# Kernel optimization log

Measured on AMD Instinct MI355X. Metric: run time of the kernel, lower is better.

## Reference

```python
import math
import jax, jax.numpy as jnp
import numpy as np

N_HEADS = 16
LOCAL_HEADS = 8
GLOBAL_HEADS = N_HEADS - LOCAL_HEADS
WINDOW = 256
NEG_INF = -1e30


def setup_inputs() -> dict:
    key = jax.random.key(0)
    ks = jax.random.split(key, 6)
    B, S, E = 1, 4096, 1024
    inp = {
        "hidden_states": jax.random.normal(ks[0], (B, S, E), dtype=jnp.float32),
        "Wq": jax.random.normal(ks[1], (E, E), dtype=jnp.float32) * (1.0 / math.sqrt(E)),
        "Wk": jax.random.normal(ks[2], (E, E), dtype=jnp.float32) * (1.0 / math.sqrt(E)),
        "Wv": jax.random.normal(ks[3], (E, E), dtype=jnp.float32) * (1.0 / math.sqrt(E)),
        "Wo": jax.random.normal(ks[4], (E, E), dtype=jnp.float32) * (1.0 / math.sqrt(E)),
        "bo": jnp.zeros((E,), dtype=jnp.float32),
    }
    return inp


def reference(hidden_states, Wq, Wk, Wv, Wo, bo):
    B, S, E = hidden_states.shape
    H, D = N_HEADS, E // N_HEADS
    scale = 1.0 / math.sqrt(D)

    def proj(W):
        # nn.Linear: x @ W.T ; reshape to [B, H, S, D]
        y = jnp.einsum('bse,fe->bsf', hidden_states, W)
        return y.reshape(B, S, H, D).transpose(0, 2, 1, 3)

    q = proj(Wq) * scale
    k = proj(Wk)
    v = proj(Wv)

    i = jnp.arange(S)[:, None]
    j = jnp.arange(S)[None, :]
    causal = j <= i                      # [S, S] allowed positions
    local = causal & (j >= i - WINDOW)   # sliding window of width WINDOW+1

    def attend(qh, kh, vh, mask):
        scores = jnp.einsum('bhsd,bhtd->bhst', qh, kh)
        scores = jnp.where(mask, scores, NEG_INF)
        w = jax.nn.softmax(scores, axis=-1)
        return jnp.einsum('bhst,bhtd->bhsd', w, vh)

    out_g = attend(q[:, :GLOBAL_HEADS], k[:, :GLOBAL_HEADS], v[:, :GLOBAL_HEADS], causal)
    out_l = attend(q[:, GLOBAL_HEADS:], k[:, GLOBAL_HEADS:], v[:, GLOBAL_HEADS:], local)

    attn = jnp.concatenate([out_g, out_l], axis=1)       # [B, H, S, D]
    attn = attn.transpose(0, 2, 1, 3).reshape(B, S, E)    # [B, S, E]
    return jnp.einsum('bse,fe->bsf', attn, Wo) + bo
```

## Files before the change

### kernel.cpp

```cpp
#include <hip/hip_runtime.h>
#include <hip/hip_fp16.h>

#define S_LEN 4096
#define EMB   1024
#define NH    16
#define HD    64
#define GH    8
#define WIN   256

typedef _Float16 half8 __attribute__((ext_vector_type(8)));
typedef float    f32x4 __attribute__((ext_vector_type(4)));
typedef unsigned short ushort8 __attribute__((ext_vector_type(8)));

static __device__ __forceinline__ f32x4 mfma16(half8 a, half8 b, f32x4 c) {
    return __builtin_amdgcn_mfma_f32_16x16x32_f16(a, b, c, 0, 0, 0);
}

#define GLOAD16(g, l) __builtin_amdgcn_global_load_lds( \
    (const __attribute__((address_space(1))) void*)(g), \
    (__attribute__((address_space(3))) void*)(l), 16, 0, 0)

__global__ __launch_bounds__(256) void split_kernel(
    const float* __restrict__ X,  const float* __restrict__ Wq, const float* __restrict__ Wk,
    const float* __restrict__ Wv, const float* __restrict__ Wo,
    __half* __restrict__ Xhi, __half* __restrict__ Xlo,
    __half* __restrict__ Wh,  __half* __restrict__ Wl,
    __half* __restrict__ Woh, __half* __restrict__ Wol)
{
    const int NT = gridDim.x * blockDim.x;
    for (int i = blockIdx.x * blockDim.x + threadIdx.x; i < 2097152; i += NT) {
        const float* src; __half *dh, *dl; int off;
        if (i < 1048576)      { src = X;  dh = Xhi;           dl = Xlo;           off = i; }
        else if (i < 1310720) { src = Wq; dh = Wh;            dl = Wl;            off = i - 1048576; }
        else if (i < 1572864) { src = Wk; dh = Wh + 1048576;  dl = Wl + 1048576;  off = i - 1310720; }
        else if (i < 1835008) { src = Wv; dh = Wh + 2097152;  dl = Wl + 2097152;  off = i - 1572864; }
        else                  { src = Wo; dh = Woh;           dl = Wol;           off = i - 1835008; }
        float4 xv = *(const float4*)(src + (size_t)off * 4);
        union { __half h[4]; uint2 u; } ph, pl;
        float xs[4] = {xv.x, xv.y, xv.z, xv.w};
        #pragma unroll
        for (int j = 0; j < 4; ++j) {
            __half hj = __float2half_rn(xs[j]);
            ph.h[j] = hj;
            pl.h[j] = __float2half_rn(xs[j] - __half2float(hj));
        }
        *(uint2*)(dh + (size_t)off * 4) = ph.u;
        *(uint2*)(dl + (size_t)off * 4) = pl.u;
    }
}

__global__ __launch_bounds__(256) void gemm_split_kernel(
    const __half* __restrict__ Ah_, const __half* __restrict__ Al_,
    const __half* __restrict__ Bh_, const __half* __restrict__ Bl_,
    int mode, __half* __restrict__ qkv_out,
    float* __restrict__ fo_out, const float* __restrict__ bias)
{
    __shared__ __align__(16) char lds[65536];
    char* LA_h = lds;
    char* LA_l = lds + 16384;
    char* LB_h = lds + 32768;
    char* LB_l = lds + 49152;

    const int tid  = threadIdx.x;
    const int w    = tid >> 6, lane = tid & 63;
    const int bm   = blockIdx.x * 128, bn = blockIdx.y * 128;
    const int wm0  = (w & 1) * 64, wn0 = (w >> 1) * 64;
    const int lr   = lane & 15;
    const int lk   = lane >> 4;

    const char *gAh[4], *gAl[4], *gBh[4], *gBl[4];
    int ldsoff[4];
    #pragma unroll
    for (int i = 0; i < 4; ++i) {
        const int c = tid + i * 256;
        const int row = c >> 3;
        const int sw  = ((c & 7) ^ (row & 7)) * 16;
        gAh[i] = (const char*)Ah_ + (size_t)(bm + row) * 2048 + sw;
        gAl[i] = (const char*)Al_ + (size_t)(bm + row) * 2048 + sw;
        gBh[i] = (const char*)Bh_ + (size_t)(bn + row) * 2048 + sw;
        gBl[i] = (const char*)Bl_ + (size_t)(bn + row) * 2048 + sw;
        ldsoff[i] = ((tid >> 6) * 64 + i * 256) * 16;
    }

    f32x4 acc[4][4];
    #pragma unroll
    for (int mi = 0; mi < 4; ++mi)
        #pragma unroll
        for (int ni = 0; ni < 4; ++ni) acc[mi][ni] = (f32x4){0.f, 0.f, 0.f, 0.f};

    for (int k0 = 0; k0 < 1024; k0 += 64) {
        __syncthreads();
        const size_t kb = (size_t)k0 * 2;
        #pragma unroll
        for (int i = 0; i < 4; ++i) {
            GLOAD16(gAh[i] + kb, LA_h + ldsoff[i]);
            GLOAD16(gAl[i] + kb, LA_l + ldsoff[i]);
            GLOAD16(gBh[i] + kb, LB_h + ldsoff[i]);
            GLOAD16(gBl[i] + kb, LB_l + ldsoff[i]);
        }
        __syncthreads();

        #pragma unroll
        for (int kh = 0; kh < 2; ++kh) {
            half8 afh[4], afl[4], bfh[4], bfl[4];
            #pragma unroll
            for (int f = 0; f < 4; ++f) {
                const int ar = wm0 + f * 16 + lr;
                const int ab = ar * 128 + ((kh * 64 + lk * 16) ^ ((ar & 7) << 4));
                afh[f] = *(const half8*)(LA_h + ab);
                afl[f] = *(const half8*)(LA_l + ab);
                const int br = wn0 + f * 16 + lr;
                const int bb = br * 128 + ((kh * 64 + lk * 16) ^ ((br & 7) << 4));
                bfh[f] = *(const half8*)(LB_h + bb);
                bfl[f] = *(const half8*)(LB_l + bb);
            }
            #pragma unroll
            for (int mi = 0; mi < 4; ++mi)
                #pragma unroll
                for (int ni = 0; ni < 4; ++ni) {
                    acc[mi][ni] = mfma16(afh[mi], bfh[ni], acc[mi][ni]);
                    acc[mi][ni] = mfma16(afh[mi], bfl[ni], acc[mi][ni]);
                    acc[mi][ni] = mfma16(afl[mi], bfh[ni], acc[mi][ni]);
                }
        }
    }

    if (mode == 0) {
        #pragma unroll
        for (int ni = 0; ni < 4; ++ni) {
            const int n  = bn + wn0 + ni * 16 + lr;
            const int hg = n >> 6;
            const int d  = n & 63;
            const float alpha = ((n >> 10) == 0) ? 0.125f : 1.0f;
            __half* base = qkv_out + (size_t)hg * S_LEN * HD + d;
            #pragma unroll
            for (int mi = 0; mi < 4; ++mi) {
                const int m = bm + wm0 + mi * 16 + lk * 4;
                #pragma unroll
                for (int r = 0; r < 4; ++r)
                    base[(size_t)(m + r) * HD] = __float2half_rn(acc[mi][ni][r] * alpha);
            }
        }
    } else {
        #pragma unroll
        for (int ni = 0; ni < 4; ++ni) {
            const int n = bn + wn0 + ni * 16 + lr;
            const float bv = bias[n];
            #pragma unroll
            for (int mi = 0; mi < 4; ++mi) {
                const int m = bm + wm0 + mi * 16 + lk * 4;
                #pragma unroll
                for (int r = 0; r < 4; ++r)
                    fo_out[(size_t)(m + r) * EMB + n] = acc[mi][ni][r] + bv;
            }
        }
    }
}

__global__ __launch_bounds__(256) void attn_mfma_kernel(
    const __half* __restrict__ q, const __half* __restrict__ k, const __half* __restrict__ v,
    __half* __restrict__ Ohi, __half* __restrict__ Olo )
{
    __shared__ __align__(16) unsigned char smem[32768];
    char* Qs = (char*)smem;
    char* Ks = (char*)smem + 8192;
    char* Vt = (char*)smem + 16384;
    char* Pl = (char*)smem + 24576;

    const int qb  = 63 - blockIdx.x;
    const int h   = blockIdx.y;
    const bool is_local = (h >= GH);
    const int tid  = threadIdx.x;
    const int w    = tid >> 6;
    const int lane = tid & 63;
    const int lq   = lane & 15;
    const int hi   = lane >> 4;

    const char* qh = (const char*)(q + (size_t)h * S_LEN * HD);
    const char* kh = (const char*)(k + (size_t)h * S_LEN * HD);
    const char* vh = (const char*)(v + (size_t)h * S_LEN * HD);

    #pragma unroll
    for (int e = 0; e < 2; ++e) {
        const int flat = e * 4096 + tid * 16;
        const int row  = flat >> 7;
        const int src  = flat ^ ((row & 7) << 4);
        *(uint4*)(Qs + flat) = *(const uint4*)(qh + (size_t)qb * 8192 + src);
    }
    __syncthreads();

    half8 qf[2];
    #pragma unroll
    for (int ks = 0; ks < 2; ++ks) {
        const int row = w * 16 + lq;
        int byte = row * 128 + hi * 16 + ks * 64;
        byte ^= (row & 7) << 4;
        qf[ks] = *(const half8*)(Qs + byte);
    }

    float m_run = -1e30f, l_run = 0.f;
    f32x4 po[4];
    #pragma unroll
    for (int i = 0; i < 4; ++i) po[i] = (f32x4){0.f, 0.f, 0.f, 0.f};

    const int qg = qb * 64 + w * 16 + lq;
    const int kt_lo = is_local ? ((qb - 4 > 0) ? qb - 4 : 0) : 0;
    char* plw = Pl + w * 2048;

    for (int kv = kt_lo; kv <= qb; ++kv) {
        __syncthreads();

        #pragma unroll
        for (int e = 0; e < 2; ++e) {
            const int flat = e * 4096 + tid * 16;
            const int row  = flat >> 7;
            const int src  = flat ^ ((row & 7) << 4);
            *(uint4*)(Ks + flat) = *(const uint4*)(kh + (size_t)kv * 8192 + src);
        }
        {
            const int j0 = (tid & 31) * 2;
            const int d0 = (tid >> 5) * 8;
            ushort8 v0 = *(const ushort8*)(vh + (size_t)(kv * 64 + j0)     * 128 + d0 * 2);
            ushort8 v1 = *(const ushort8*)(vh + (size_t)(kv * 64 + j0 + 1) * 128 + d0 * 2);
            #pragma unroll
            for (int i = 0; i < 8; ++i) {
                const int d = d0 + i;
                int byte = d * 128 + j0 * 2;
                byte ^= (d & 7) << 4;
                *(unsigned int*)(Vt + byte) = (unsigned int)v0[i] | ((unsigned int)v1[i] << 16);
            }
        }
        __syncthreads();

        f32x4 st[4];
        #pragma unroll
        for (int i = 0; i < 4; ++i) st[i] = (f32x4){0.f, 0.f, 0.f, 0.f};
        #pragma unroll
        for (int ks = 0; ks < 2; ++ks) {
            #pragma unroll
            for (int kt = 0; kt < 4; ++kt) {
                const int row = kt * 16 + lq;
                int byte = row * 128 + hi * 16 + ks * 64;
                byte ^= (row & 7) << 4;
                half8 kf = *(const half8*)(Ks + byte);
                st[kt] = mfma16(kf, qf[ks], st[kt]);
            }
        }

        float mx = -1e30f;
        #pragma unroll
        for (int kt = 0; kt < 4; ++kt)
            #pragma unroll
            for (int r = 0; r < 4; ++r) {
                const int kg = kv * 64 + kt * 16 + hi * 4 + r;
                const bool ok = (kg <= qg) && (!is_local || (kg + WIN >= qg));
                const float s = ok ? st[kt][r] : -1e30f;
                st[kt][r] = s;
                mx = fmaxf(mx, s);
            }
        mx = fmaxf(mx, __shfl_xor(mx, 16));
        mx = fmaxf(mx, __shfl_xor(mx, 32));
        const float mnew  = fmaxf(m_run, mx);
        const float scale = __expf(m_run - mnew);
        float lsum = 0.f;
        #pragma unroll
        for (int kt = 0; kt < 4; ++kt)
            #pragma unroll
            for (int r = 0; r < 4; ++r) {
                const float p = __expf(st[kt][r] - mnew);
                st[kt][r] = p;
                lsum += p;
            }
        lsum += __shfl_xor(lsum, 16);
        lsum += __shfl_xor(lsum, 32);
        l_run = l_run * scale + lsum;
        m_run = mnew;
        #pragma unroll
        for (int dt = 0; dt < 4; ++dt)
            #pragma unroll
            for (int r = 0; r < 4; ++r) po[dt][r] *= scale;

        #pragma unroll
        for (int kt = 0; kt < 4; ++kt) {
            int byte = lq * 128 + kt * 32 + hi * 8;
            byte ^= (lq & 7) << 4;
            union { __half2 h2[2]; uint2 u; } pu;
            pu.h2[0] = __floats2half2_rn(st[kt][0], st[kt][1]);
            pu.h2[1] = __floats2half2_rn(st[kt][2], st[kt][3]);
            *(uint2*)(plw + byte) = pu.u;
        }

        #pragma unroll
        for (int ks = 0; ks < 2; ++ks) {
            int pbyte = lq * 128 + ks * 64 + hi * 16;
            pbyte ^= (lq & 7) << 4;
            half8 pf = *(const half8*)(plw + pbyte);
            #pragma unroll
            for (int dt = 0; dt < 4; ++dt) {
                const int drow = dt * 16 + lq;
                int vbyte = drow * 128 + ks * 64 + hi * 16;
                vbyte ^= (drow & 7) << 4;
                half8 vf = *(const half8*)(Vt + vbyte);
                po[dt] = mfma16(vf, pf, po[dt]);
            }
        }
    }

    const float linv = 1.0f / l_run;
    __half* oh = Ohi + (size_t)qg * EMB + h * HD;
    __half* ol = Olo + (size_t)qg * EMB + h * HD;
    #pragma unroll
    for (int dt = 0; dt < 4; ++dt)
        #pragma unroll
        for (int r = 0; r < 4; ++r) {
            const float vfull = po[dt][r] * linv;
            const __half vhi = __float2half_rn(vfull);
            oh[dt * 16 + hi * 4 + r] = vhi;
            ol[dt * 16 + hi * 4 + r] = __float2half_rn(vfull - __half2float(vhi));
        }
}

extern "C" void kernel_launch(void* const* d_in, const int* in_sizes, int n_in,
                              void* d_out, int out_size, void* d_ws, size_t ws_size,
                              hipStream_t stream) {
    const float* X  = (const float*)d_in[0];
    const float* Wq = (const float*)d_in[1];
    const float* Wk = (const float*)d_in[2];
    const float* Wv = (const float*)d_in[3];
    const float* Wo = (const float*)d_in[4];
    const float* bo = (const float*)d_in[5];
    float* out = (float*)d_out;

    __half* ws   = (__half*)d_ws;
    __half* qkvb = ws;
    __half* XOhi = ws + 12582912;
    __half* XOlo = ws + 16777216;
    __half* Wh   = ws + 20971520;
    __half* Wl   = ws + 24117248;
    __half* Woh  = ws + 27262976;
    __half* Wol  = ws + 28311552;

    split_kernel<<<dim3(2048), 256, 0, stream>>>(X, Wq, Wk, Wv, Wo,
                                                 XOhi, XOlo, Wh, Wl, Woh, Wol);
    gemm_split_kernel<<<dim3(32, 24), 256, 0, stream>>>(XOhi, XOlo, Wh, Wl,
                                                        0, qkvb, nullptr, nullptr);
    attn_mfma_kernel<<<dim3(64, 16), 256, 0, stream>>>(qkvb, qkvb + 4194304, qkvb + 8388608,
                                                       XOhi, XOlo);
    gemm_split_kernel<<<dim3(32, 8), 256, 0, stream>>>(XOhi, XOlo, Woh, Wol,
                                                       1, nullptr, out, bo);
}
```

Measured before the change: 311.2 us.

## Split causal global-head attention across KV chunks with a combine pass

Global causal heads are now processed split-KV style: query blocks beyond the first 16 get their KV range cut into chunks of 16 tiles, and each chunk is handled by its own workgroup that writes unnormalized partial outputs plus running max and sum. A new combine kernel merges the partials with log-sum-exp weights and writes the hi/lo fp16 output. Local heads share the same grid and write directly. This evens out the work per block so long causal rows no longer bound the kernel tail, at the cost of an extra launch, fp32 partial traffic, and workspace reuse that overlaps the QKV weight buffers.

New measurement: 262.9 us. 15.5% less time.

```diff
diff --git a/kernel.cpp b/kernel.cpp
--- a/kernel.cpp
+++ b/kernel.cpp
@@ -157,9 +157,10 @@
     }
 }
 
-__global__ __launch_bounds__(256) void attn_mfma_kernel(
+__global__ __launch_bounds__(256) void attn_pass1(
     const __half* __restrict__ q, const __half* __restrict__ k, const __half* __restrict__ v,
-    __half* __restrict__ Ohi, __half* __restrict__ Olo )
+    __half* __restrict__ Ohi, __half* __restrict__ Olo,
+    float* __restrict__ partO, float* __restrict__ partML)
 {
     __shared__ __align__(16) unsigned char smem[32768];
     char* Qs = (char*)smem;
@@ -167,9 +168,30 @@
     char* Vt = (char*)smem + 16384;
     char* Pl = (char*)smem + 24576;
 
-    const int qb  = 63 - blockIdx.x;
-    const int h   = blockIdx.y;
-    const bool is_local = (h >= GH);
+    int h, qb, kt_lo, kt_hi, pslot = 0;
+    bool is_local, direct;
+    if (blockIdx.x < 160) {
+        h = blockIdx.y;
+        is_local = false;
+        const int i = 159 - blockIdx.x;
+        int c;
+        if (i < 16)      { qb = i;                c = 0; }
+        else if (i < 48) { const int t = i - 16;  qb = 16 + (t >> 1); c = t & 1; }
+        else if (i < 96) { const int t = i - 48;  qb = 32 + t / 3;    c = t % 3; }
+        else             { const int t = i - 96;  qb = 48 + (t >> 2); c = t & 3; }
+        kt_lo = c * 16;
+        kt_hi = (kt_lo + 15 < qb) ? kt_lo + 15 : qb;
+        direct = (qb < 16);
+        pslot  = (h * 48 + (qb - 16)) * 4 + c;
+    } else {
+        h  = 8 + blockIdx.y;
+        qb = blockIdx.x - 160;
+        is_local = true;
+        kt_lo = (qb - 4 > 0) ? qb - 4 : 0;
+        kt_hi = qb;
+        direct = true;
+    }
+
     const int tid  = threadIdx.x;
     const int w    = tid >> 6;
     const int lane = tid & 63;
@@ -204,10 +226,9 @@
     for (int i = 0; i < 4; ++i) po[i] = (f32x4){0.f, 0.f, 0.f, 0.f};
 
     const int qg = qb * 64 + w * 16 + lq;
-    const int kt_lo = is_local ? ((qb - 4 > 0) ? qb - 4 : 0) : 0;
     char* plw = Pl + w * 2048;
 
-    for (int kv = kt_lo; kv <= qb; ++kv) {
+    for (int kv = kt_lo; kv <= kt_hi; ++kv) {
         __syncthreads();
 
         #pragma unroll
@@ -306,18 +327,91 @@
         }
     }
 
-    const float linv = 1.0f / l_run;
-    __half* oh = Ohi + (size_t)qg * EMB + h * HD;
-    __half* ol = Olo + (size_t)qg * EMB + h * HD;
-    #pragma unroll
-    for (int dt = 0; dt < 4; ++dt)
-        #pragma unroll
-        for (int r = 0; r < 4; ++r) {
-            const float vfull = po[dt][r] * linv;
-            const __half vhi = __float2half_rn(vfull);
-            oh[dt * 16 + hi * 4 + r] = vhi;
-            ol[dt * 16 + hi * 4 + r] = __float2half_rn(vfull - __half2float(vhi));
-        }
+    if (direct) {
+        const float linv = 1.0f / l_run;
+        __half* oh = Ohi + (size_t)qg * EMB + h * HD;
+        __half* ol = Olo + (size_t)qg * EMB + h * HD;
+        #pragma unroll
+        for (int dt = 0; dt < 4; ++dt)
+            #pragma unroll
+            for (int r = 0; r < 4; ++r) {
+                const float vfull = po[dt][r] * linv;
+                const __half vhi = __float2half_rn(vfull);
+                oh[dt * 16 + hi * 4 + r] = vhi;
+                ol[dt * 16 + hi * 4 + r] = __float2half_rn(vfull - __half2float(vhi));
+            }
+    } else {
+        float* op = partO + (size_t)pslot * 4096 + (w * 16 + lq) * 64;
+        #pragma unroll
+        for (int dt = 0; dt < 4; ++dt)
+            #pragma unroll
+            for (int r = 0; r < 4; ++r)
+                op[dt * 16 + hi * 4 + r] = po[dt][r];
+        if (hi == 0) {
+            partML[(size_t)pslot * 128 + (w * 16 + lq) * 2]     = m_run;
+            partML[(size_t)pslot * 128 + (w * 16 + lq) * 2 + 1] = l_run;
+        }
+    }
+}
+
+__global__ __launch_bounds__(256) void attn_combine(
+    const float* __restrict__ partO, const float* __restrict__ partML,
+    __half* __restrict__ Ohi, __half* __restrict__ Olo)
+{
+    const int qb = 16 + blockIdx.x;
+    const int h  = blockIdx.y;
+    const int nc = (qb >> 4) + 1;
+    const int row = threadIdx.x >> 2;
+    const int d0  = (threadIdx.x & 3) * 16;
+    const int base_slot = (h * 48 + (qb - 16)) * 4;
+
+    float M = -1e30f, mv[4], lv[4];
+    #pragma unroll
+    for (int i = 0; i < 4; ++i)
+        if (i < nc) {
+            mv[i] = partML[(size_t)(base_slot + i) * 128 + row * 2];
+            lv[i] = partML[(size_t)(base_slot + i) * 128 + row * 2 + 1];
+            M = fmaxf(M, mv[i]);
+        }
+    float L = 0.f, wgt[4];
+    #pragma unroll
+    for (int i = 0; i < 4; ++i)
+        if (i < nc) {
+            wgt[i] = __expf(mv[i] - M);
+            L += lv[i] * wgt[i];
+        }
+
+    float o[16];
+    #pragma unroll
+    for (int j = 0; j < 16; ++j) o[j] = 0.f;
+    #pragma unroll
+    for (int i = 0; i < 4; ++i)
+        if (i < nc) {
+            const float* src = partO + (size_t)(base_slot + i) * 4096 + row * 64 + d0;
+            const float wi = wgt[i];
+            #pragma unroll
+            for (int j4 = 0; j4 < 4; ++j4) {
+                float4 s4 = *(const float4*)(src + j4 * 4);
+                o[j4*4+0] = fmaf(wi, s4.x, o[j4*4+0]);
+                o[j4*4+1] = fmaf(wi, s4.y, o[j4*4+1]);
+                o[j4*4+2] = fmaf(wi, s4.z, o[j4*4+2]);
+                o[j4*4+3] = fmaf(wi, s4.w, o[j4*4+3]);
+            }
+        }
+    const float Linv = 1.0f / L;
+    ushort8 ph[2], pl[2];
+    #pragma unroll
+    for (int j = 0; j < 16; ++j) {
+        const float vfull = o[j] * Linv;
+        const __half vhi = __float2half_rn(vfull);
+        ph[j >> 3][j & 7] = __half_as_ushort(vhi);
+        pl[j >> 3][j & 7] = __half_as_ushort(__float2half_rn(vfull - __half2float(vhi)));
+    }
+    const size_t ob = (size_t)(qb * 64 + row) * EMB + h * HD + d0;
+    *(ushort8*)((__half*)Ohi + ob)     = ph[0];
+    *(ushort8*)((__half*)Ohi + ob + 8) = ph[1];
+    *(ushort8*)((__half*)Olo + ob)     = pl[0];
+    *(ushort8*)((__half*)Olo + ob + 8) = pl[1];
 }
 
 extern "C" void kernel_launch(void* const* d_in, const int* in_sizes, int n_in,
@@ -335,17 +429,20 @@
     __half* qkvb = ws;
     __half* XOhi = ws + 12582912;
     __half* XOlo = ws + 16777216;
-    __half* Wh   = ws + 20971520;
-    __half* Wl   = ws + 24117248;
-    __half* Woh  = ws + 27262976;
-    __half* Wol  = ws + 28311552;
+    __half* Woh  = ws + 20971520;
+    __half* Wol  = ws + 22020096;
+    __half* Wh   = ws + 23068672;
+    __half* Wl   = ws + 26214400;
+    float* partO  = (float*)(ws + 23068672);
+    float* partML = partO + 6291456;
 
     split_kernel<<<dim3(2048), 256, 0, stream>>>(X, Wq, Wk, Wv, Wo,
                                                  XOhi, XOlo, Wh, Wl, Woh, Wol);
     gemm_split_kernel<<<dim3(32, 24), 256, 0, stream>>>(XOhi, XOlo, Wh, Wl,
                                                         0, qkvb, nullptr, nullptr);
-    attn_mfma_kernel<<<dim3(64, 16), 256, 0, stream>>>(qkvb, qkvb + 4194304, qkvb + 8388608,
-                                                       XOhi, XOlo);
+    attn_pass1<<<dim3(224, 8), 256, 0, stream>>>(qkvb, qkvb + 4194304, qkvb + 8388608,
+                                                 XOhi, XOlo, partO, partML);
+    attn_combine<<<dim3(48, 8), 256, 0, stream>>>(partO, partML, XOhi, XOlo);
     gemm_split_kernel<<<dim3(32, 8), 256, 0, stream>>>(XOhi, XOlo, Woh, Wol,
                                                        1, nullptr, out, bo);
 }
```
